# Kernel optimization log

Measured on AMD Instinct MI355X. Metric: run time of the kernel, lower is better.

## Reference

```python
import jax, jax.numpy as jnp
import numpy as np

NUM_MODES = 64
NUM_KNOTS = 8
NUM_STEPS = 80
B = 8192


def setup_inputs() -> dict:
    key = jax.random.key(0)
    k1, k2, k3, k4, k5 = jax.random.split(key, 5)
    inputs = jax.random.normal(k1, (B, NUM_MODES + NUM_MODES * NUM_KNOTS * 2), dtype=jnp.float32)
    x = jax.random.normal(k2, (B, 1), dtype=jnp.float32)
    y = jax.random.normal(k3, (B, 1), dtype=jnp.float32)
    yaw = jax.random.normal(k4, (B, 1), dtype=jnp.float32)
    centroids = jax.random.normal(k5, (NUM_MODES, NUM_STEPS * 2), dtype=jnp.float32)
    return {"inputs": inputs, "x": x, "y": y, "yaw": yaw, "centroids": centroids}


def _cubic_bspline_basis(t):
    # t in [0,1); tensorflow_graphics cubic B-spline basis, shape t.shape + (4,)
    t2 = t * t
    t3 = t2 * t
    b0 = (1.0 - t) ** 3 / 6.0
    b1 = (3.0 * t3 - 6.0 * t2 + 4.0) / 6.0
    b2 = (-3.0 * t3 + 3.0 * t2 + 3.0 * t + 1.0) / 6.0
    b3 = t3 / 6.0
    return jnp.stack([b0, b1, b2, b3], axis=-1)


def reference(inputs, x, y, yaw, centroids):
    M, C, T = NUM_MODES, NUM_KNOTS, NUM_STEPS
    confidences = jax.nn.softmax(inputs[:, :M], axis=-1)  # (B, M)
    knots = inputs[:, M:].reshape(-1, M, 2, C)  # (B, M, 2, C)

    # positions = arange(0, C-3, (C-3)/T) -> T values in [0, C-3)
    max_pos = float(C - 3)
    pos = jnp.arange(T, dtype=knots.dtype) * (max_pos / T)  # (T,)
    shift = jnp.floor(pos).astype(jnp.int32)  # (T,)
    basis = _cubic_bspline_basis(pos - shift)  # (T, 4)

    # sparse gather of the 4 active knots per position (equivalent to full
    # num_knots weight vector in tfg.bspline.interpolate, non-cyclical)
    idx = shift[:, None] + jnp.arange(4, dtype=jnp.int32)[None, :]  # (T, 4)
    gathered = knots[..., idx]  # (B, M, 2, T, 4)
    spline = jnp.einsum('bmdtk,tk->bmtd', gathered, basis)  # (B, M, T, 2)

    pred = spline + centroids.reshape(1, M, T, 2)  # centroid bias

    c = jnp.cos(yaw)  # (B, 1)
    s = jnp.sin(yaw)
    flat = pred.reshape(-1, M * T, 2)
    px = c * flat[..., 0] - s * flat[..., 1] + x
    py = s * flat[..., 0] + c * flat[..., 1] + y
    pred = jnp.stack([px, py], axis=-1).reshape(-1, M, T, 2)
    return pred, confidences, knots
```

## Files before the change

### kernel.cpp

```cpp
#include <hip/hip_runtime.h>
#include <math.h>

#define NMODES 64
#define NKNOTS 8
#define NSTEPS 80
#define ROW    1088
#define ROW4   272
#define PREDF  10240
#define VECS   2560

__device__ __forceinline__ void eval_pair(const float* __restrict__ s_kn,
                                          int m, int t, float cx, float cy,
                                          float rc, float rs, float X, float Y,
                                          float& px, float& py)
{
    float pos = (float)t * 0.0625f;
    int   sh  = (int)pos;
    float tt  = pos - (float)sh;
    float tt2 = tt * tt;
    float tt3 = tt2 * tt;
    const float inv6 = 1.0f / 6.0f;
    float omt = 1.0f - tt;
    float b0 = omt * omt * omt * inv6;
    float b1 = (3.0f * tt3 - 6.0f * tt2 + 4.0f) * inv6;
    float b2 = (-3.0f * tt3 + 3.0f * tt2 + 3.0f * tt + 1.0f) * inv6;
    float b3 = tt3 * inv6;
    const float2* k = (const float2*)(s_kn + m * 16 + sh * 2);
    float2 k0 = k[0], k1 = k[1], k2 = k[2], k3 = k[3];
    float fx = b0 * k0.x + b1 * k1.x + b2 * k2.x + b3 * k3.x + cx;
    float fy = b0 * k0.y + b1 * k1.y + b2 * k2.y + b3 * k3.y + cy;
    px = rc * fx - rs * fy + X;
    py = rs * fx + rc * fy + Y;
}

__launch_bounds__(256, 4)
__global__ void head_kernel(const float* __restrict__ inputs,
                            const float* __restrict__ x,
                            const float* __restrict__ y,
                            const float* __restrict__ yaw,
                            const float* __restrict__ centroids,
                            float* __restrict__ pred,
                            float* __restrict__ conf,
                            float* __restrict__ knots_out)
{
    __shared__ float s_in[ROW];
    __shared__ float s_kn[NMODES * NKNOTS * 2];
    __shared__ float s_rot[4];

    const int tid = threadIdx.x;
    const int b   = blockIdx.x;

    const float4* row4  = (const float4*)(inputs + (size_t)b * ROW);
    float4*       s_in4 = (float4*)s_in;
    s_in4[tid] = row4[tid];
    if (tid < ROW4 - 256) s_in4[256 + tid] = row4[256 + tid];

    if (tid == 0) {
        float sy, cy;
        sincosf(yaw[b], &sy, &cy);
        s_rot[0] = cy;
        s_rot[1] = sy;
        s_rot[2] = x[b];
        s_rot[3] = y[b];
    }
    __syncthreads();

    float4 kv = s_in4[16 + tid];
    ((float4*)(knots_out + (size_t)b * 1024))[tid] = kv;

    {
        int g = tid * 4;
        const float* kvp = (const float*)&kv;
        #pragma unroll
        for (int e = 0; e < 4; ++e) {
            int gg = g + e;
            int m  = gg >> 4;
            int r  = gg & 15;
            int d  = r >> 3;
            int c  = r & 7;
            s_kn[(m << 4) + (c << 1) + d] = kvp[e];
        }
    }

    if (tid < 64) {
        float v  = s_in[tid];
        float mx = v;
        #pragma unroll
        for (int off = 32; off > 0; off >>= 1)
            mx = fmaxf(mx, __shfl_xor(mx, off));
        float e = expf(v - mx);
        float sum = e;
        #pragma unroll
        for (int off = 32; off > 0; off >>= 1)
            sum += __shfl_xor(sum, off);
        conf[(size_t)b * NMODES + tid] = e / sum;
    }
    __syncthreads();

    const float rc = s_rot[0], rs = s_rot[1], X = s_rot[2], Y = s_rot[3];
    const float4* cent4 = (const float4*)centroids;
    float4* out4 = (float4*)(pred + (size_t)b * PREDF);

    #pragma unroll
    for (int j = 0; j < VECS / 256; ++j) {
        int idx = j * 256 + tid;
        int m   = idx / 40;
        int t0  = (idx - m * 40) * 2;
        float4 cent = cent4[idx];
        float4 o;
        eval_pair(s_kn, m, t0,     cent.x, cent.y, rc, rs, X, Y, o.x, o.y);
        eval_pair(s_kn, m, t0 + 1, cent.z, cent.w, rc, rs, X, Y, o.z, o.w);
        out4[idx] = o;
    }
}

extern "C" void kernel_launch(void* const* d_in, const int* in_sizes, int n_in,
                              void* d_out, int out_size, void* d_ws, size_t ws_size,
                              hipStream_t stream)
{
    const float* inputs    = (const float*)d_in[0];
    const float* x         = (const float*)d_in[1];
    const float* y         = (const float*)d_in[2];
    const float* yaw       = (const float*)d_in[3];
    const float* centroids = (const float*)d_in[4];

    const int B = in_sizes[1];

    float* pred      = (float*)d_out;
    float* conf      = pred + (size_t)B * NMODES * NSTEPS * 2;
    float* knots_out = conf + (size_t)B * NMODES;

    head_kernel<<<B, 256, 0, stream>>>(inputs, x, y, yaw, centroids,
                                       pred, conf, knots_out);
}
```

Baseline: 407.5 us.

## Map four threads per mode with register-resident knots, drop shared transpose

Replaces the shared-memory knot transpose and its second barrier with a per-thread assignment: each group of four threads handles one mode and loads that mode's 16 knot values straight from the staged input row into registers. Spline shifts and fractional offsets become compile-time constants per step, which removes the integer division and the dynamic LDS gathers. Writes now go to strided positions within each mode's segment (stride of four float4s), which may slightly reduce store coalescing, and the extra knot registers raise per-thread register use.

Measured after the change: 480.1 us. 1.18x slower.

```diff
diff --git a/kernel.cpp b/kernel.cpp
--- a/kernel.cpp
+++ b/kernel.cpp
@@ -7,31 +7,6 @@
 #define ROW    1088
 #define ROW4   272
 #define PREDF  10240
-#define VECS   2560
-
-__device__ __forceinline__ void eval_pair(const float* __restrict__ s_kn,
-                                          int m, int t, float cx, float cy,
-                                          float rc, float rs, float X, float Y,
-                                          float& px, float& py)
-{
-    float pos = (float)t * 0.0625f;
-    int   sh  = (int)pos;
-    float tt  = pos - (float)sh;
-    float tt2 = tt * tt;
-    float tt3 = tt2 * tt;
-    const float inv6 = 1.0f / 6.0f;
-    float omt = 1.0f - tt;
-    float b0 = omt * omt * omt * inv6;
-    float b1 = (3.0f * tt3 - 6.0f * tt2 + 4.0f) * inv6;
-    float b2 = (-3.0f * tt3 + 3.0f * tt2 + 3.0f * tt + 1.0f) * inv6;
-    float b3 = tt3 * inv6;
-    const float2* k = (const float2*)(s_kn + m * 16 + sh * 2);
-    float2 k0 = k[0], k1 = k[1], k2 = k[2], k3 = k[3];
-    float fx = b0 * k0.x + b1 * k1.x + b2 * k2.x + b3 * k3.x + cx;
-    float fy = b0 * k0.y + b1 * k1.y + b2 * k2.y + b3 * k3.y + cy;
-    px = rc * fx - rs * fy + X;
-    py = rs * fx + rc * fy + Y;
-}
 
 __launch_bounds__(256, 4)
 __global__ void head_kernel(const float* __restrict__ inputs,
@@ -44,7 +19,6 @@
                             float* __restrict__ knots_out)
 {
     __shared__ float s_in[ROW];
-    __shared__ float s_kn[NMODES * NKNOTS * 2];
     __shared__ float s_rot[4];
 
     const int tid = threadIdx.x;
@@ -65,22 +39,7 @@
     }
     __syncthreads();
 
-    float4 kv = s_in4[16 + tid];
-    ((float4*)(knots_out + (size_t)b * 1024))[tid] = kv;
-
-    {
-        int g = tid * 4;
-        const float* kvp = (const float*)&kv;
-        #pragma unroll
-        for (int e = 0; e < 4; ++e) {
-            int gg = g + e;
-            int m  = gg >> 4;
-            int r  = gg & 15;
-            int d  = r >> 3;
-            int c  = r & 7;
-            s_kn[(m << 4) + (c << 1) + d] = kvp[e];
-        }
-    }
+    ((float4*)(knots_out + (size_t)b * 1024))[tid] = s_in4[16 + tid];
 
     if (tid < 64) {
         float v  = s_in[tid];
@@ -95,23 +54,64 @@
             sum += __shfl_xor(sum, off);
         conf[(size_t)b * NMODES + tid] = e / sum;
     }
-    __syncthreads();
+
+    const int m = tid >> 2;
+    const int q = tid & 3;
+    float kx[8], ky[8];
+    {
+        const float4* kn4 = (const float4*)(s_in + NMODES + m * 16);
+        float4 a0 = kn4[0], a1 = kn4[1], a2 = kn4[2], a3 = kn4[3];
+        kx[0] = a0.x; kx[1] = a0.y; kx[2] = a0.z; kx[3] = a0.w;
+        kx[4] = a1.x; kx[5] = a1.y; kx[6] = a1.z; kx[7] = a1.w;
+        ky[0] = a2.x; ky[1] = a2.y; ky[2] = a2.z; ky[3] = a2.w;
+        ky[4] = a3.x; ky[5] = a3.y; ky[6] = a3.z; ky[7] = a3.w;
+    }
 
     const float rc = s_rot[0], rs = s_rot[1], X = s_rot[2], Y = s_rot[3];
+    const float qf = (float)q * 0.125f;
     const float4* cent4 = (const float4*)centroids;
     float4* out4 = (float4*)(pred + (size_t)b * PREDF);
+    const int colbase = m * 40 + q;
 
-    #pragma unroll
-    for (int j = 0; j < VECS / 256; ++j) {
-        int idx = j * 256 + tid;
-        int m   = idx / 40;
-        int t0  = (idx - m * 40) * 2;
-        float4 cent = cent4[idx];
-        float4 o;
-        eval_pair(s_kn, m, t0,     cent.x, cent.y, rc, rs, X, Y, o.x, o.y);
-        eval_pair(s_kn, m, t0 + 1, cent.z, cent.w, rc, rs, X, Y, o.z, o.w);
-        out4[idx] = o;
+#define BSPLINE_PAIR(U, SH, CX, CY, OX, OY)                                   \
+    {                                                                         \
+        float u  = (U);                                                       \
+        float u2 = u * u, u3 = u2 * u, omu = 1.0f - u;                        \
+        float b0 = omu * omu * omu * (1.0f / 6.0f);                           \
+        float b1 = (3.0f * u3 - 6.0f * u2 + 4.0f) * (1.0f / 6.0f);            \
+        float b2 = (-3.0f * u3 + 3.0f * u2 + 3.0f * u + 1.0f) * (1.0f/6.0f);  \
+        float b3 = u3 * (1.0f / 6.0f);                                        \
+        float fx = b0 * kx[SH] + b1 * kx[(SH)+1] + b2 * kx[(SH)+2] +          \
+                   b3 * kx[(SH)+3] + (CX);                                    \
+        float fy = b0 * ky[SH] + b1 * ky[(SH)+1] + b2 * ky[(SH)+2] +          \
+                   b3 * ky[(SH)+3] + (CY);                                    \
+        (OX) = rc * fx - rs * fy + X;                                         \
+        (OY) = rs * fx + rc * fy + Y;                                         \
     }
+
+#define STEP(I, SH, TB)                                                       \
+    {                                                                         \
+        const int idx = colbase + (I) * 4;                                    \
+        float4 cent = cent4[idx];                                             \
+        float4 o;                                                             \
+        BSPLINE_PAIR((TB) + qf,            SH, cent.x, cent.y, o.x, o.y);     \
+        BSPLINE_PAIR((TB) + qf + 0.0625f,  SH, cent.z, cent.w, o.z, o.w);     \
+        out4[idx] = o;                                                        \
+    }
+
+    STEP(0, 0, 0.0f)
+    STEP(1, 0, 0.5f)
+    STEP(2, 1, 0.0f)
+    STEP(3, 1, 0.5f)
+    STEP(4, 2, 0.0f)
+    STEP(5, 2, 0.5f)
+    STEP(6, 3, 0.0f)
+    STEP(7, 3, 0.5f)
+    STEP(8, 4, 0.0f)
+    STEP(9, 4, 0.5f)
+
+#undef STEP
+#undef BSPLINE_PAIR
 }
 
 extern "C" void kernel_launch(void* const* d_in, const int* in_sizes, int n_in,
```

## Drop shared input staging, use nontemporal stores and incremental index math

Applied to the files above, without the earlier changes.

Knots are loaded straight from global memory into registers and written out, with no staging of the full input row in shared memory. This removes one barrier, and softmax reads its logits directly from global memory. All outputs now use nontemporal stores so the large pred stream does not pollute the cache. The spline loop replaces per-iteration division by 40 with incremental mode/step counters and simplified basis constants, and uses partial unrolling. This trades some register pressure and cache behaviour for less shared traffic and fewer integer ops in a store-bound kernel.

Result: no change. 403.8 us (-0.9%).

```diff
diff --git a/kernel.cpp b/kernel.cpp
--- a/kernel.cpp
+++ b/kernel.cpp
@@ -5,33 +5,9 @@
 #define NKNOTS 8
 #define NSTEPS 80
 #define ROW    1088
-#define ROW4   272
 #define PREDF  10240
-#define VECS   2560
 
-__device__ __forceinline__ void eval_pair(const float* __restrict__ s_kn,
-                                          int m, int t, float cx, float cy,
-                                          float rc, float rs, float X, float Y,
-                                          float& px, float& py)
-{
-    float pos = (float)t * 0.0625f;
-    int   sh  = (int)pos;
-    float tt  = pos - (float)sh;
-    float tt2 = tt * tt;
-    float tt3 = tt2 * tt;
-    const float inv6 = 1.0f / 6.0f;
-    float omt = 1.0f - tt;
-    float b0 = omt * omt * omt * inv6;
-    float b1 = (3.0f * tt3 - 6.0f * tt2 + 4.0f) * inv6;
-    float b2 = (-3.0f * tt3 + 3.0f * tt2 + 3.0f * tt + 1.0f) * inv6;
-    float b3 = tt3 * inv6;
-    const float2* k = (const float2*)(s_kn + m * 16 + sh * 2);
-    float2 k0 = k[0], k1 = k[1], k2 = k[2], k3 = k[3];
-    float fx = b0 * k0.x + b1 * k1.x + b2 * k2.x + b3 * k3.x + cx;
-    float fy = b0 * k0.y + b1 * k1.y + b2 * k2.y + b3 * k3.y + cy;
-    px = rc * fx - rs * fy + X;
-    py = rs * fx + rc * fy + Y;
-}
+typedef float f4 __attribute__((ext_vector_type(4)));
 
 __launch_bounds__(256, 4)
 __global__ void head_kernel(const float* __restrict__ inputs,
@@ -43,47 +19,37 @@
                             float* __restrict__ conf,
                             float* __restrict__ knots_out)
 {
-    __shared__ float s_in[ROW];
     __shared__ float s_kn[NMODES * NKNOTS * 2];
     __shared__ float s_rot[4];
 
     const int tid = threadIdx.x;
     const int b   = blockIdx.x;
 
-    const float4* row4  = (const float4*)(inputs + (size_t)b * ROW);
-    float4*       s_in4 = (float4*)s_in;
-    s_in4[tid] = row4[tid];
-    if (tid < ROW4 - 256) s_in4[256 + tid] = row4[256 + tid];
+    const f4* row4 = (const f4*)(inputs + (size_t)b * ROW);
+    f4 kv = row4[16 + tid];
+    __builtin_nontemporal_store(kv, (f4*)(knots_out + (size_t)b * 1024) + tid);
+    {
+        int g = tid * 4;
+        #pragma unroll
+        for (int e = 0; e < 4; ++e) {
+            int gg = g + e;
+            int m  = gg >> 4;
+            int rr = gg & 15;
+            int d  = rr >> 3;
+            int c  = rr & 7;
+            s_kn[(m << 4) + (c << 1) + d] = kv[e];
+        }
+    }
 
     if (tid == 0) {
         float sy, cy;
         sincosf(yaw[b], &sy, &cy);
-        s_rot[0] = cy;
-        s_rot[1] = sy;
-        s_rot[2] = x[b];
-        s_rot[3] = y[b];
-    }
-    __syncthreads();
-
-    float4 kv = s_in4[16 + tid];
-    ((float4*)(knots_out + (size_t)b * 1024))[tid] = kv;
-
-    {
-        int g = tid * 4;
-        const float* kvp = (const float*)&kv;
-        #pragma unroll
-        for (int e = 0; e < 4; ++e) {
-            int gg = g + e;
-            int m  = gg >> 4;
-            int r  = gg & 15;
-            int d  = r >> 3;
-            int c  = r & 7;
-            s_kn[(m << 4) + (c << 1) + d] = kvp[e];
-        }
+        s_rot[0] = cy;  s_rot[1] = sy;
+        s_rot[2] = x[b]; s_rot[3] = y[b];
     }
 
     if (tid < 64) {
-        float v  = s_in[tid];
+        float v  = inputs[(size_t)b * ROW + tid];
         float mx = v;
         #pragma unroll
         for (int off = 32; off > 0; off >>= 1)
@@ -93,24 +59,57 @@
         #pragma unroll
         for (int off = 32; off > 0; off >>= 1)
             sum += __shfl_xor(sum, off);
-        conf[(size_t)b * NMODES + tid] = e / sum;
+        __builtin_nontemporal_store(e / sum, conf + (size_t)b * NMODES + tid);
     }
+
     __syncthreads();
 
     const float rc = s_rot[0], rs = s_rot[1], X = s_rot[2], Y = s_rot[3];
-    const float4* cent4 = (const float4*)centroids;
-    float4* out4 = (float4*)(pred + (size_t)b * PREDF);
+    const f4* cent4 = (const f4*)centroids;
+    f4* out4 = (f4*)(pred + (size_t)b * PREDF);
 
-    #pragma unroll
-    for (int j = 0; j < VECS / 256; ++j) {
-        int idx = j * 256 + tid;
-        int m   = idx / 40;
-        int t0  = (idx - m * 40) * 2;
-        float4 cent = cent4[idx];
-        float4 o;
-        eval_pair(s_kn, m, t0,     cent.x, cent.y, rc, rs, X, Y, o.x, o.y);
-        eval_pair(s_kn, m, t0 + 1, cent.z, cent.w, rc, rs, X, Y, o.z, o.w);
-        out4[idx] = o;
+    int m   = (tid * 205) >> 13;
+    int r   = tid - m * 40;
+    int idx = tid;
+
+    #pragma unroll 2
+    for (int j = 0; j < 10; ++j) {
+        const int   sh = r >> 3;
+        const float u0 = (float)(r & 7) * 0.125f;
+        const float u1 = u0 + 0.0625f;
+
+        const float2* kp = (const float2*)(s_kn + (m << 4) + (sh << 1));
+        float2 k0 = kp[0], k1 = kp[1], k2 = kp[2], k3 = kp[3];
+
+        f4 cent = cent4[idx];
+        f4 o;
+        {
+            float u2 = u0 * u0, u3 = u2 * u0, omu = 1.0f - u0;
+            float b0 = omu * omu * omu * (1.0f / 6.0f);
+            float b1 = 0.5f * u3 - u2 + (2.0f / 3.0f);
+            float b2 = -0.5f * u3 + 0.5f * u2 + 0.5f * u0 + (1.0f / 6.0f);
+            float b3 = u3 * (1.0f / 6.0f);
+            float fx = b0 * k0.x + b1 * k1.x + b2 * k2.x + b3 * k3.x + cent.x;
+            float fy = b0 * k0.y + b1 * k1.y + b2 * k2.y + b3 * k3.y + cent.y;
+            o.x = rc * fx - rs * fy + X;
+            o.y = rs * fx + rc * fy + Y;
+        }
+        {
+            float u2 = u1 * u1, u3 = u2 * u1, omu = 1.0f - u1;
+            float b0 = omu * omu * omu * (1.0f / 6.0f);
+            float b1 = 0.5f * u3 - u2 + (2.0f / 3.0f);
+            float b2 = -0.5f * u3 + 0.5f * u2 + 0.5f * u1 + (1.0f / 6.0f);
+            float b3 = u3 * (1.0f / 6.0f);
+            float fx = b0 * k0.x + b1 * k1.x + b2 * k2.x + b3 * k3.x + cent.z;
+            float fy = b0 * k0.y + b1 * k1.y + b2 * k2.y + b3 * k3.y + cent.w;
+            o.z = rc * fx - rs * fy + X;
+            o.w = rs * fx + rc * fy + Y;
+        }
+        __builtin_nontemporal_store(o, out4 + idx);
+
+        idx += 256;
+        r += 16; m += 6;
+        if (r >= 40) { r -= 40; ++m; }
     }
 }
 
```
